# Kernel optimization log

Hardware: AMD Instinct MI355X
Metric: run time of the kernel (lower is better)

## Reference

```python
import jax, jax.numpy as jnp
import numpy as np

S, D, H, DK, DV = 4096, 1024, 16, 64, 64


def setup_inputs() -> dict:
    key = jax.random.key(0)
    ks = jax.random.split(key, 6)
    x = jax.random.normal(ks[0], (S, D), dtype=jnp.float32)
    # per-head projection weights, stacked over heads; scaled for numerical sanity
    Wq = jax.random.normal(ks[1], (H, D, DK), dtype=jnp.float32) / np.sqrt(D)
    Wk = jax.random.normal(ks[2], (H, D, DK), dtype=jnp.float32) / np.sqrt(D)
    Wv = jax.random.normal(ks[3], (H, D, DV), dtype=jnp.float32) / np.sqrt(D)
    Wc = jax.random.normal(ks[4], (H * DV, D), dtype=jnp.float32) / np.sqrt(H * DV)
    bc = jnp.zeros((D,), dtype=jnp.float32)
    return {"x": x, "Wq": Wq, "Wk": Wk, "Wv": Wv, "Wc": Wc, "bc": bc}


def reference(x, Wq, Wk, Wv, Wc, bc):
    # Per-head projections (original loops over heads with separate Linears;
    # stacking over h is the same math, vectorized).
    q = jnp.einsum("sd,hdk->hsk", x, Wq)   # [H,S,DK]
    k = jnp.einsum("sd,hdk->hsk", x, Wk)   # [H,S,DK]
    v = jnp.einsum("sd,hdv->hsv", x, Wv)   # [H,S,DV]
    scores = jnp.einsum("hsk,htk->hst", q, k) / jnp.sqrt(jnp.asarray(DK, x.dtype))
    probs = jax.nn.softmax(scores, axis=-1)  # softmax over last dim, per row
    o = jnp.einsum("hst,htv->hsv", probs, v)  # [H,S,DV]
    cat = jnp.transpose(o, (1, 0, 2)).reshape(S, H * DV)  # concat heads on last dim
    return cat @ Wc + bc  # output projection with bias
```

## Files before the change

kernel.cpp:

```cpp
#include <hip/hip_runtime.h>
#include <hip/hip_bf16.h>

#define S_ 4096
#define D_ 1024
#define H_ 16
#define DK_ 64
#define DV_ 64

typedef short bf16x8 __attribute__((ext_vector_type(8)));
typedef short bf16x4 __attribute__((ext_vector_type(4)));
typedef float floatx4 __attribute__((ext_vector_type(4)));
using bf16 = __hip_bfloat16;

#define MFMA16(a, b, c) __builtin_amdgcn_mfma_f32_16x16x32_bf16(a, b, c, 0, 0, 0)

#if __has_builtin(__builtin_amdgcn_exp2f)
#define EXP2(x) __builtin_amdgcn_exp2f(x)
#else
#define EXP2(x) exp2f(x)
#endif

__device__ __forceinline__ void stage16(const void* g, void* l) {
    __builtin_amdgcn_global_load_lds(
        (const __attribute__((address_space(1))) void*)g,
        (__attribute__((address_space(3))) void*)l, 16, 0, 0);
}

__device__ __forceinline__ bf16x8 ldsfrag(const bf16* base, int row, int chunk) {
    return *(const bf16x8*)(base + row * 64 + (((chunk ^ (row & 7))) << 3));
}
__device__ __forceinline__ bf16x8 ldsfrag32(const bf16* base, int row, int chunk) {
    return *(const bf16x8*)(base + row * 32 + (((chunk ^ (row & 3))) << 3));
}

__device__ __forceinline__ unsigned short bfbits(float f) {
    union { bf16 h; unsigned short u; } c; c.h = __float2bfloat16(f); return c.u;
}

__global__ __launch_bounds__(256)
void prep(const float* __restrict__ x, const float* __restrict__ Wq,
          const float* __restrict__ Wk, const float* __restrict__ Wv,
          const float* __restrict__ Wc,
          bf16* __restrict__ xb, bf16* __restrict__ Wt, bf16* __restrict__ Wct)
{
    __shared__ float ls[64][65];
    const int bx = blockIdx.x, t = threadIdx.x;

    if (bx < 2048) {
        int i = bx * 2048 + t * 8;
        float4 a = *(const float4*)(x + i);
        float4 b = *(const float4*)(x + i + 4);
        ushort4 lo, hi;
        lo.x = bfbits(a.x); lo.y = bfbits(a.y); lo.z = bfbits(a.z); lo.w = bfbits(a.w);
        hi.x = bfbits(b.x); hi.y = bfbits(b.y); hi.z = bfbits(b.z); hi.w = bfbits(b.w);
        *(ushort4*)(xb + i) = lo;
        *(ushort4*)(xb + i + 4) = hi;
        return;
    }
    if (bx < 2816) {
        const int idx = bx - 2048;
        const int z = idx >> 4, which = z >> 4, h = z & 15;
        const float* s = (which == 0 ? Wq : which == 1 ? Wk : Wv) + (size_t)h * D_ * 64;
        bf16* d = Wt + ((size_t)which * 1024 + h * 64) * D_;
        const float scale = (which == 0) ? 0.125f * 1.44269504088896340736f : 1.0f;
        const int r0 = (idx & 15) * 64;
        {
            int r = t >> 2, cseg = (t & 3) * 16;
            const float* sp = s + (size_t)(r0 + r) * 64 + cseg;
            #pragma unroll
            for (int i = 0; i < 16; i += 4) {
                float4 v = *(const float4*)(sp + i);
                ls[r][cseg + i + 0] = v.x; ls[r][cseg + i + 1] = v.y;
                ls[r][cseg + i + 2] = v.z; ls[r][cseg + i + 3] = v.w;
            }
        }
        __syncthreads();
        {
            int c = t >> 2, rseg = (t & 3) * 16;
            bf16* dp = d + (size_t)c * D_ + r0 + rseg;
            #pragma unroll
            for (int i = 0; i < 16; i++) dp[i] = __float2bfloat16(ls[rseg + i][c] * scale);
        }
        return;
    }
    {
        const int idx = bx - 2816;
        const int r0 = (idx & 15) * 64, c0 = (idx >> 4) * 64;
        {
            int r = t >> 2, cseg = (t & 3) * 16;
            const float* sp = Wc + (size_t)(r0 + r) * D_ + c0 + cseg;
            #pragma unroll
            for (int i = 0; i < 16; i += 4) {
                float4 v = *(const float4*)(sp + i);
                ls[r][cseg + i + 0] = v.x; ls[r][cseg + i + 1] = v.y;
                ls[r][cseg + i + 2] = v.z; ls[r][cseg + i + 3] = v.w;
            }
        }
        __syncthreads();
        {
            int c = t >> 2, rseg = (t & 3) * 16;
            bf16* dp = Wct + (size_t)(c0 + c) * D_ + r0 + rseg;
            #pragma unroll
            for (int i = 0; i < 16; i++) dp[i] = __float2bfloat16(ls[rseg + i][c]);
        }
    }
}

__global__ __launch_bounds__(256)
void qkv_gemm(const bf16* __restrict__ xb, const bf16* __restrict__ Wt,
              bf16* __restrict__ Qb, bf16* __restrict__ Kb, bf16* __restrict__ Vtb)
{
    const int m0 = blockIdx.x * 128;
    const int n0 = blockIdx.y * 128;
    __shared__ __align__(16) bf16 xa[2][128 * 32];
    __shared__ __align__(16) bf16 wb2[2][128 * 32];

    const int t = threadIdx.x, lane = t & 63, w = t >> 6;
    const int l15 = lane & 15, quad = lane >> 4;

    auto stage_a = [&](int buf, int kk) {
        #pragma unroll
        for (int j = 0; j < 2; j++) {
            int row = j * 64 + (t >> 2);
            int ch  = (t & 3) ^ (row & 3);
            stage16((const char*)xb + ((size_t)(m0 + row) * D_ + kk) * 2 + ch * 16,
                    (char*)&xa[buf][0] + (j * 4 + w) * 1024);
        }
    };
    auto stage_b = [&](int buf, int kk) {
        #pragma unroll
        for (int j = 0; j < 2; j++) {
            int row = j * 64 + (t >> 2);
            int ch  = (t & 3) ^ (row & 3);
            stage16((const char*)Wt + ((size_t)(n0 + row) * D_ + kk) * 2 + ch * 16,
                    (char*)&wb2[buf][0] + (j * 4 + w) * 1024);
        }
    };

    const floatx4 fz = {0.f, 0.f, 0.f, 0.f};
    floatx4 acc[2][8];
    #pragma unroll
    for (int mt = 0; mt < 2; mt++)
        #pragma unroll
        for (int nt = 0; nt < 8; nt++) acc[mt][nt] = fz;

    stage_a(0, 0); stage_b(0, 0);
    for (int kt = 0; kt < 32; kt++) {
        int cur = kt & 1;
        __syncthreads();
        if (kt < 31) { stage_a(cur ^ 1, (kt + 1) * 32); stage_b(cur ^ 1, (kt + 1) * 32); }
        bf16x8 a0 = ldsfrag32(&xa[cur][0], w * 32 + l15,      quad);
        bf16x8 a1 = ldsfrag32(&xa[cur][0], w * 32 + 16 + l15, quad);
        #pragma unroll
        for (int nt = 0; nt < 8; nt++) {
            bf16x8 b = ldsfrag32(&wb2[cur][0], nt * 16 + l15, quad);
            acc[0][nt] = MFMA16(a0, b, acc[0][nt]);
            acc[1][nt] = MFMA16(a1, b, acc[1][nt]);
        }
    }

    const int which = n0 >> 10;
    #pragma unroll
    for (int nt = 0; nt < 8; nt++) {
        int n = n0 + nt * 16 + l15;
        int hh = (n >> 6) & 15, col = n & 63;
        #pragma unroll
        for (int mt = 0; mt < 2; mt++)
            #pragma unroll
            for (int r = 0; r < 4; r++) {
                int s = m0 + w * 32 + mt * 16 + quad * 4 + r;
                bf16 val = __float2bfloat16(acc[mt][nt][r]);
                if (which == 0)      Qb[((size_t)hh * S_ + s) * 64 + col] = val;
                else if (which == 1) Kb[((size_t)hh * S_ + s) * 64 + col] = val;
                else                 Vtb[((size_t)hh * 64 + col) * S_ + s] = val;
            }
    }
}

template<int NKT, bool FULL>
__global__ __launch_bounds__(256, 4)
void attn(const bf16* __restrict__ Qb, const bf16* __restrict__ Kb,
          const bf16* __restrict__ Vtb, bf16* __restrict__ Cat,
          float* __restrict__ Opart, float* __restrict__ lpart)
{
    const int m0 = blockIdx.x * 128;
    const int h  = blockIdx.y;
    const int half = blockIdx.z;
    const int keybase = half * (NKT * 64);

    __shared__ __align__(16) bf16 ka[2][64 * 64];
    __shared__ __align__(16) bf16 vt[2][64 * 64];

    const int t = threadIdx.x, lane = t & 63, w = t >> 6;
    const int l15 = lane & 15, quad = lane >> 4;

    auto stage_kv = [&](int buf, int key0) {
        const char* kg = (const char*)(Kb + ((size_t)h * S_ + key0) * 64);
        #pragma unroll
        for (int j = 0; j < 2; j++) {
            int c = (j * 4 + w) * 64 + lane;
            int row = c >> 3, ch = (c & 7) ^ (row & 7);
            stage16(kg + row * 128 + ch * 16, (char*)&ka[buf][0] + (j * 4 + w) * 1024);
        }
        const char* vg = (const char*)(Vtb + (size_t)h * 64 * S_ + key0);
        #pragma unroll
        for (int j = 0; j < 2; j++) {
            int c = (j * 4 + w) * 64 + lane;
            int row = c >> 3, ch = (c & 7) ^ (row & 7);
            stage16(vg + (size_t)row * (S_ * 2) + ch * 16, (char*)&vt[buf][0] + (j * 4 + w) * 1024);
        }
    };

    bf16x8 qf[2][2];
    #pragma unroll
    for (int nq = 0; nq < 2; nq++)
        #pragma unroll
        for (int ks = 0; ks < 2; ks++)
            qf[nq][ks] = *(const bf16x8*)(Qb +
                ((size_t)h * S_ + m0 + w * 32 + nq * 16 + l15) * 64 + ks * 32 + quad * 8);

    const floatx4 fz = {0.f, 0.f, 0.f, 0.f};
    floatx4 acc[2][4];
    float rs[2] = {0.f, 0.f};
    #pragma unroll
    for (int nq = 0; nq < 2; nq++)
        #pragma unroll
        for (int nt = 0; nt < 4; nt++) acc[nq][nt] = fz;

    stage_kv(0, keybase);
    __syncthreads();

    for (int kt = 0; kt < NKT; kt++) {
        const int cur = kt & 1;
        if (kt + 1 < NKT) stage_kv(cur ^ 1, keybase + (kt + 1) * 64);

        floatx4 sc[4][2];
        #pragma unroll
        for (int mk = 0; mk < 4; mk++)
            #pragma unroll
            for (int nq = 0; nq < 2; nq++) sc[mk][nq] = fz;
        #pragma unroll
        for (int ks = 0; ks < 2; ks++) {
            bf16x8 af[4];
            #pragma unroll
            for (int mk = 0; mk < 4; mk++)
                af[mk] = ldsfrag(&ka[cur][0], mk * 16 + l15, ks * 4 + quad);
            #pragma unroll
            for (int mk = 0; mk < 4; mk++)
                #pragma unroll
                for (int nq = 0; nq < 2; nq++)
                    sc[mk][nq] = MFMA16(af[mk], qf[nq][ks], sc[mk][nq]);
        }

        bf16x4 pf[4][2];
        #pragma unroll
        for (int mk = 0; mk < 4; mk++)
            #pragma unroll
            for (int nq = 0; nq < 2; nq++) {
                float p0 = EXP2(sc[mk][nq][0]);
                float p1 = EXP2(sc[mk][nq][1]);
                float p2 = EXP2(sc[mk][nq][2]);
                float p3 = EXP2(sc[mk][nq][3]);
                rs[nq] += (p0 + p1) + (p2 + p3);
                union { bf16x4 v; unsigned short e[4]; } u;
                u.e[0] = bfbits(p0); u.e[1] = bfbits(p1);
                u.e[2] = bfbits(p2); u.e[3] = bfbits(p3);
                pf[mk][nq] = u.v;
            }

        #pragma unroll
        for (int p = 0; p < 2; p++) {
            union { bf16x8 v8; bf16x4 v4[2]; } b8[2];
            #pragma unroll
            for (int nq = 0; nq < 2; nq++) {
                b8[nq].v4[0] = pf[2 * p + 0][nq];
                b8[nq].v4[1] = pf[2 * p + 1][nq];
            }
            #pragma unroll
            for (int nt = 0; nt < 4; nt++) {
                const char* vb = (const char*)&vt[cur][0]
                               + (nt * 16 + l15) * 128 + (quad & 1) * 8;
                const int r7 = l15 & 7;
                union { bf16x8 v8; bf16x4 v4[2]; } a8;
                a8.v4[0] = *(const bf16x4*)(vb + (((4 * p +     (quad >> 1)) ^ r7) << 4));
                a8.v4[1] = *(const bf16x4*)(vb + (((4 * p + 2 + (quad >> 1)) ^ r7) << 4));
                #pragma unroll
                for (int nq = 0; nq < 2; nq++)
                    acc[nq][nt] = MFMA16(a8.v8, b8[nq].v8, acc[nq][nt]);
            }
        }
        __syncthreads();
    }

    #pragma unroll
    for (int nq = 0; nq < 2; nq++) {
        rs[nq] += __shfl_xor(rs[nq], 16);
        rs[nq] += __shfl_xor(rs[nq], 32);
    }

    if (FULL) {
        #pragma unroll
        for (int nq = 0; nq < 2; nq++) {
            float inv = 1.0f / rs[nq];
            int q = m0 + w * 32 + nq * 16 + l15;
            #pragma unroll
            for (int nt = 0; nt < 4; nt++) {
                ushort4 o;
                o.x = bfbits(acc[nq][nt][0] * inv);
                o.y = bfbits(acc[nq][nt][1] * inv);
                o.z = bfbits(acc[nq][nt][2] * inv);
                o.w = bfbits(acc[nq][nt][3] * inv);
                *(ushort4*)(Cat + (size_t)q * (H_ * DV_) + h * 64 + nt * 16 + quad * 4) = o;
            }
        }
    } else {
        const size_t plane = (size_t)(half * H_ + h) * S_;
        #pragma unroll
        for (int nq = 0; nq < 2; nq++) {
            int q = m0 + w * 32 + nq * 16 + l15;
            #pragma unroll
            for (int nt = 0; nt < 4; nt++) {
                float4 o = { acc[nq][nt][0], acc[nq][nt][1],
                             acc[nq][nt][2], acc[nq][nt][3] };
                *(float4*)(Opart + (plane + q) * 64 + nt * 16 + quad * 4) = o;
            }
            if (quad == 0) lpart[plane + q] = rs[nq];
        }
    }
}

__global__ __launch_bounds__(256)
void combine(const float* __restrict__ Opart, const float* __restrict__ lpart,
             bf16* __restrict__ Cat)
{
    const int h = blockIdx.y;
    const int off = blockIdx.x * 1024 + threadIdx.x * 4;
    const int s = off >> 6, dv = off & 63;
    float4 o0 = *(const float4*)(Opart + (size_t)h * S_ * 64 + off);
    float4 o1 = *(const float4*)(Opart + (size_t)(H_ + h) * S_ * 64 + off);
    float inv = 1.0f / (lpart[(size_t)h * S_ + s] + lpart[(size_t)(H_ + h) * S_ + s]);
    ushort4 o;
    o.x = bfbits((o0.x + o1.x) * inv);
    o.y = bfbits((o0.y + o1.y) * inv);
    o.z = bfbits((o0.z + o1.z) * inv);
    o.w = bfbits((o0.w + o1.w) * inv);
    *(ushort4*)(Cat + (size_t)s * (H_ * DV_) + h * 64 + dv) = o;
}

__global__ __launch_bounds__(256)
void out_proj(const bf16* __restrict__ Cat, const bf16* __restrict__ Wct,
              const float* __restrict__ bc, float* __restrict__ out)
{
    const int m0 = blockIdx.x * 128;
    const int n0 = blockIdx.y * 64;
    __shared__ __align__(16) bf16 ca[2][128 * 32];
    __shared__ __align__(16) bf16 wb2[2][64 * 32];

    const int t = threadIdx.x, lane = t & 63, w = t >> 6;
    const int l15 = lane & 15, quad = lane >> 4;

    auto stage_a = [&](int buf, int kk) {
        #pragma unroll
        for (int j = 0; j < 2; j++) {
            int row = j * 64 + (t >> 2);
            int ch  = (t & 3) ^ (row & 3);
            stage16((const char*)Cat + ((size_t)(m0 + row) * D_ + kk) * 2 + ch * 16,
                    (char*)&ca[buf][0] + (j * 4 + w) * 1024);
        }
    };
    auto stage_b = [&](int buf, int kk) {
        int row = t >> 2;
        int ch  = (t & 3) ^ (row & 3);
        stage16((const char*)Wct + ((size_t)(n0 + row) * D_ + kk) * 2 + ch * 16,
                (char*)&wb2[buf][0] + w * 1024);
    };

    const floatx4 fz = {0.f, 0.f, 0.f, 0.f};
    floatx4 acc[2][4];
    #pragma unroll
    for (int mt = 0; mt < 2; mt++)
        #pragma unroll
        for (int nt = 0; nt < 4; nt++) acc[mt][nt] = fz;

    stage_a(0, 0); stage_b(0, 0);
    for (int kt = 0; kt < 32; kt++) {
        int cur = kt & 1;
        __syncthreads();
        if (kt < 31) { stage_a(cur ^ 1, (kt + 1) * 32); stage_b(cur ^ 1, (kt + 1) * 32); }
        bf16x8 a0 = ldsfrag32(&ca[cur][0], w * 32 + l15,      quad);
        bf16x8 a1 = ldsfrag32(&ca[cur][0], w * 32 + 16 + l15, quad);
        #pragma unroll
        for (int nt = 0; nt < 4; nt++) {
            bf16x8 b = ldsfrag32(&wb2[cur][0], nt * 16 + l15, quad);
            acc[0][nt] = MFMA16(a0, b, acc[0][nt]);
            acc[1][nt] = MFMA16(a1, b, acc[1][nt]);
        }
    }

    #pragma unroll
    for (int nt = 0; nt < 4; nt++) {
        int col = n0 + nt * 16 + l15;
        float bias = bc[col];
        #pragma unroll
        for (int mt = 0; mt < 2; mt++)
            #pragma unroll
            for (int r = 0; r < 4; r++) {
                int row = m0 + w * 32 + mt * 16 + quad * 4 + r;
                out[(size_t)row * D_ + col] = acc[mt][nt][r] + bias;
            }
    }
}

extern "C" void kernel_launch(void* const* d_in, const int* in_sizes, int n_in,
                              void* d_out, int out_size, void* d_ws, size_t ws_size,
                              hipStream_t stream)
{
    const float* x  = (const float*)d_in[0];
    const float* Wq = (const float*)d_in[1];
    const float* Wk = (const float*)d_in[2];
    const float* Wv = (const float*)d_in[3];
    const float* Wc = (const float*)d_in[4];
    const float* bc = (const float*)d_in[5];
    float* out = (float*)d_out;

    bf16* xb  = (bf16*)d_ws;
    bf16* Cat = xb;
    bf16* Wt  = xb  + (size_t)S_ * D_;
    bf16* Wct = Wt  + (size_t)3 * H_ * 64 * D_;
    bf16* Qb  = Wct + (size_t)D_ * H_ * DV_;
    bf16* Kb  = Qb  + (size_t)H_ * S_ * 64;
    bf16* Vtb = Kb  + (size_t)H_ * S_ * 64;
    float* Opart = (float*)(Vtb + (size_t)H_ * 64 * S_);
    float* lpart = Opart + (size_t)2 * H_ * S_ * 64;

    const size_t need_split = (size_t)((char*)(lpart + (size_t)2 * H_ * S_) - (char*)d_ws);
    const bool split = ws_size >= need_split;

    prep<<<dim3(3072), 256, 0, stream>>>(x, Wq, Wk, Wv, Wc, xb, Wt, Wct);
    qkv_gemm<<<dim3(S_ / 128, 3072 / 128), 256, 0, stream>>>(xb, Wt, Qb, Kb, Vtb);

    if (split) {
        attn<32, false><<<dim3(S_ / 128, H_, 2), 256, 0, stream>>>(
            Qb, Kb, Vtb, Cat, Opart, lpart);
        combine<<<dim3(S_ * 64 / 1024, H_), 256, 0, stream>>>(Opart, lpart, Cat);
    } else {
        attn<64, true><<<dim3(S_ / 128, H_, 1), 256, 0, stream>>>(
            Qb, Kb, Vtb, Cat, Opart, lpart);
    }

    out_proj<<<dim3(S_ / 128, D_ / 64), 256, 0, stream>>>(Cat, Wct, bc, out);
}
```

Measured before the change: 241.3 us.

## Store split-attention partials in bf16, pack conversions, precompute LDS offsets

The split-key attention partial outputs are now written as bf16 instead of fp32, which halves the Opart traffic between attn and combine. The combine kernel is widened to 8 elements per thread to match. Scalar bf16 conversions are replaced with packed two-element conversions in prep, attn and combine. Per-iteration LDS swizzle offsets are precomputed once, and the zero-initialised score accumulators are folded into the first MFMA. Rounding the unnormalised partials to bf16 adds some error before the final sum.

```diff
diff --git a/kernel.cpp b/kernel.cpp
--- a/kernel.cpp
+++ b/kernel.cpp
@@ -36,6 +36,12 @@
 __device__ __forceinline__ unsigned short bfbits(float f) {
     union { bf16 h; unsigned short u; } c; c.h = __float2bfloat16(f); return c.u;
 }
+__device__ __forceinline__ float bf2f(bf16 h) { return __bfloat162float(h); }
+__device__ __forceinline__ unsigned int pkbf(float a, float b) {
+    union { __hip_bfloat162 h2; unsigned int u; } c;
+    c.h2 = __float22bfloat162_rn(float2{a, b});
+    return c.u;
+}
 
 __global__ __launch_bounds__(256)
 void prep(const float* __restrict__ x, const float* __restrict__ Wq,
@@ -50,11 +56,10 @@
         int i = bx * 2048 + t * 8;
         float4 a = *(const float4*)(x + i);
         float4 b = *(const float4*)(x + i + 4);
-        ushort4 lo, hi;
-        lo.x = bfbits(a.x); lo.y = bfbits(a.y); lo.z = bfbits(a.z); lo.w = bfbits(a.w);
-        hi.x = bfbits(b.x); hi.y = bfbits(b.y); hi.z = bfbits(b.z); hi.w = bfbits(b.w);
-        *(ushort4*)(xb + i) = lo;
-        *(ushort4*)(xb + i + 4) = hi;
+        uint4 o;
+        o.x = pkbf(a.x, a.y); o.y = pkbf(a.z, a.w);
+        o.z = pkbf(b.x, b.y); o.w = pkbf(b.z, b.w);
+        *(uint4*)(xb + i) = o;
         return;
     }
     if (bx < 2816) {
@@ -181,7 +186,7 @@
 __global__ __launch_bounds__(256, 4)
 void attn(const bf16* __restrict__ Qb, const bf16* __restrict__ Kb,
           const bf16* __restrict__ Vtb, bf16* __restrict__ Cat,
-          float* __restrict__ Opart, float* __restrict__ lpart)
+          bf16* __restrict__ Opart, float* __restrict__ lpart)
 {
     const int m0 = blockIdx.x * 128;
     const int h  = blockIdx.y;
@@ -219,6 +224,27 @@
             qf[nq][ks] = *(const bf16x8*)(Qb +
                 ((size_t)h * S_ + m0 + w * 32 + nq * 16 + l15) * 64 + ks * 32 + quad * 8);
 
+    int ka_off[8];
+    #pragma unroll
+    for (int ks = 0; ks < 2; ks++)
+        #pragma unroll
+        for (int mk = 0; mk < 4; mk++) {
+            int row = mk * 16 + l15, ch = ks * 4 + quad;
+            ka_off[ks * 4 + mk] = row * 128 + (((ch ^ (row & 7))) << 4);
+        }
+    int vt_off[2][4][2];
+    {
+        const int r7 = l15 & 7;
+        #pragma unroll
+        for (int p = 0; p < 2; p++)
+            #pragma unroll
+            for (int nt = 0; nt < 4; nt++) {
+                int base = (nt * 16 + l15) * 128 + (quad & 1) * 8;
+                vt_off[p][nt][0] = base + (((4 * p +     (quad >> 1)) ^ r7) << 4);
+                vt_off[p][nt][1] = base + (((4 * p + 2 + (quad >> 1)) ^ r7) << 4);
+            }
+    }
+
     const floatx4 fz = {0.f, 0.f, 0.f, 0.f};
     floatx4 acc[2][4];
     float rs[2] = {0.f, 0.f};
@@ -234,25 +260,26 @@
         const int cur = kt & 1;
         if (kt + 1 < NKT) stage_kv(cur ^ 1, keybase + (kt + 1) * 64);
 
+        const char* kab = (const char*)&ka[cur][0];
+        const char* vtb = (const char*)&vt[cur][0];
+
         floatx4 sc[4][2];
-        #pragma unroll
-        for (int mk = 0; mk < 4; mk++)
-            #pragma unroll
-            for (int nq = 0; nq < 2; nq++) sc[mk][nq] = fz;
         #pragma unroll
         for (int ks = 0; ks < 2; ks++) {
             bf16x8 af[4];
             #pragma unroll
             for (int mk = 0; mk < 4; mk++)
-                af[mk] = ldsfrag(&ka[cur][0], mk * 16 + l15, ks * 4 + quad);
+                af[mk] = *(const bf16x8*)(kab + ka_off[ks * 4 + mk]);
             #pragma unroll
             for (int mk = 0; mk < 4; mk++)
                 #pragma unroll
                 for (int nq = 0; nq < 2; nq++)
-                    sc[mk][nq] = MFMA16(af[mk], qf[nq][ks], sc[mk][nq]);
-        }
-
-        bf16x4 pf[4][2];
+                    sc[mk][nq] = MFMA16(af[mk], qf[nq][ks],
+                                        ks == 0 ? fz : sc[mk][nq]);
+        }
+
+        union bf4u { bf16x4 v; unsigned int u[2]; };
+        bf4u pf[4][2];
         #pragma unroll
         for (int mk = 0; mk < 4; mk++)
             #pragma unroll
@@ -262,10 +289,8 @@
                 float p2 = EXP2(sc[mk][nq][2]);
                 float p3 = EXP2(sc[mk][nq][3]);
                 rs[nq] += (p0 + p1) + (p2 + p3);
-                union { bf16x4 v; unsigned short e[4]; } u;
-                u.e[0] = bfbits(p0); u.e[1] = bfbits(p1);
-                u.e[2] = bfbits(p2); u.e[3] = bfbits(p3);
-                pf[mk][nq] = u.v;
+                pf[mk][nq].u[0] = pkbf(p0, p1);
+                pf[mk][nq].u[1] = pkbf(p2, p3);
             }
 
         #pragma unroll
@@ -273,17 +298,14 @@
             union { bf16x8 v8; bf16x4 v4[2]; } b8[2];
             #pragma unroll
             for (int nq = 0; nq < 2; nq++) {
-                b8[nq].v4[0] = pf[2 * p + 0][nq];
-                b8[nq].v4[1] = pf[2 * p + 1][nq];
+                b8[nq].v4[0] = pf[2 * p + 0][nq].v;
+                b8[nq].v4[1] = pf[2 * p + 1][nq].v;
             }
             #pragma unroll
             for (int nt = 0; nt < 4; nt++) {
-                const char* vb = (const char*)&vt[cur][0]
-                               + (nt * 16 + l15) * 128 + (quad & 1) * 8;
-                const int r7 = l15 & 7;
                 union { bf16x8 v8; bf16x4 v4[2]; } a8;
-                a8.v4[0] = *(const bf16x4*)(vb + (((4 * p +     (quad >> 1)) ^ r7) << 4));
-                a8.v4[1] = *(const bf16x4*)(vb + (((4 * p + 2 + (quad >> 1)) ^ r7) << 4));
+                a8.v4[0] = *(const bf16x4*)(vtb + vt_off[p][nt][0]);
+                a8.v4[1] = *(const bf16x4*)(vtb + vt_off[p][nt][1]);
                 #pragma unroll
                 for (int nq = 0; nq < 2; nq++)
                     acc[nq][nt] = MFMA16(a8.v8, b8[nq].v8, acc[nq][nt]);
@@ -305,12 +327,10 @@
             int q = m0 + w * 32 + nq * 16 + l15;
             #pragma unroll
             for (int nt = 0; nt < 4; nt++) {
-                ushort4 o;
-                o.x = bfbits(acc[nq][nt][0] * inv);
-                o.y = bfbits(acc[nq][nt][1] * inv);
-                o.z = bfbits(acc[nq][nt][2] * inv);
-                o.w = bfbits(acc[nq][nt][3] * inv);
-                *(ushort4*)(Cat + (size_t)q * (H_ * DV_) + h * 64 + nt * 16 + quad * 4) = o;
+                uint2 o;
+                o.x = pkbf(acc[nq][nt][0] * inv, acc[nq][nt][1] * inv);
+                o.y = pkbf(acc[nq][nt][2] * inv, acc[nq][nt][3] * inv);
+                *(uint2*)(Cat + (size_t)q * (H_ * DV_) + h * 64 + nt * 16 + quad * 4) = o;
             }
         }
     } else {
@@ -320,9 +340,10 @@
             int q = m0 + w * 32 + nq * 16 + l15;
             #pragma unroll
             for (int nt = 0; nt < 4; nt++) {
-                float4 o = { acc[nq][nt][0], acc[nq][nt][1],
-                             acc[nq][nt][2], acc[nq][nt][3] };
-                *(float4*)(Opart + (plane + q) * 64 + nt * 16 + quad * 4) = o;
+                uint2 o;
+                o.x = pkbf(acc[nq][nt][0], acc[nq][nt][1]);
+                o.y = pkbf(acc[nq][nt][2], acc[nq][nt][3]);
+                *(uint2*)(Opart + (plane + q) * 64 + nt * 16 + quad * 4) = o;
             }
             if (quad == 0) lpart[plane + q] = rs[nq];
         }
@@ -330,21 +351,22 @@
 }
 
 __global__ __launch_bounds__(256)
-void combine(const float* __restrict__ Opart, const float* __restrict__ lpart,
+void combine(const bf16* __restrict__ Opart, const float* __restrict__ lpart,
              bf16* __restrict__ Cat)
 {
     const int h = blockIdx.y;
-    const int off = blockIdx.x * 1024 + threadIdx.x * 4;
+    const int off = (blockIdx.x * 256 + threadIdx.x) * 8;
     const int s = off >> 6, dv = off & 63;
-    float4 o0 = *(const float4*)(Opart + (size_t)h * S_ * 64 + off);
-    float4 o1 = *(const float4*)(Opart + (size_t)(H_ + h) * S_ * 64 + off);
+    union { bf16x8 v; bf16 e[8]; } o0, o1;
+    o0.v = *(const bf16x8*)(Opart + (size_t)h * S_ * 64 + off);
+    o1.v = *(const bf16x8*)(Opart + (size_t)(H_ + h) * S_ * 64 + off);
     float inv = 1.0f / (lpart[(size_t)h * S_ + s] + lpart[(size_t)(H_ + h) * S_ + s]);
-    ushort4 o;
-    o.x = bfbits((o0.x + o1.x) * inv);
-    o.y = bfbits((o0.y + o1.y) * inv);
-    o.z = bfbits((o0.z + o1.z) * inv);
-    o.w = bfbits((o0.w + o1.w) * inv);
-    *(ushort4*)(Cat + (size_t)s * (H_ * DV_) + h * 64 + dv) = o;
+    uint4 o;
+    o.x = pkbf((bf2f(o0.e[0]) + bf2f(o1.e[0])) * inv, (bf2f(o0.e[1]) + bf2f(o1.e[1])) * inv);
+    o.y = pkbf((bf2f(o0.e[2]) + bf2f(o1.e[2])) * inv, (bf2f(o0.e[3]) + bf2f(o1.e[3])) * inv);
+    o.z = pkbf((bf2f(o0.e[4]) + bf2f(o1.e[4])) * inv, (bf2f(o0.e[5]) + bf2f(o1.e[5])) * inv);
+    o.w = pkbf((bf2f(o0.e[6]) + bf2f(o1.e[6])) * inv, (bf2f(o0.e[7]) + bf2f(o1.e[7])) * inv);
+    *(uint4*)(Cat + (size_t)s * (H_ * DV_) + h * 64 + dv) = o;
 }
 
 __global__ __launch_bounds__(256)
@@ -430,8 +452,8 @@
     bf16* Qb  = Wct + (size_t)D_ * H_ * DV_;
     bf16* Kb  = Qb  + (size_t)H_ * S_ * 64;
     bf16* Vtb = Kb  + (size_t)H_ * S_ * 64;
-    float* Opart = (float*)(Vtb + (size_t)H_ * 64 * S_);
-    float* lpart = Opart + (size_t)2 * H_ * S_ * 64;
+    bf16* Opart = Vtb + (size_t)H_ * 64 * S_;
+    float* lpart = (float*)(Opart + (size_t)2 * H_ * S_ * 64);
 
     const size_t need_split = (size_t)((char*)(lpart + (size_t)2 * H_ * S_) - (char*)d_ws);
     const bool split = ws_size >= need_split;
@@ -442,7 +464,7 @@
     if (split) {
         attn<32, false><<<dim3(S_ / 128, H_, 2), 256, 0, stream>>>(
             Qb, Kb, Vtb, Cat, Opart, lpart);
-        combine<<<dim3(S_ * 64 / 1024, H_), 256, 0, stream>>>(Opart, lpart, Cat);
+        combine<<<dim3(S_ * 64 / 2048, H_), 256, 0, stream>>>(Opart, lpart, Cat);
     } else {
         attn<64, true><<<dim3(S_ / 128, H_, 1), 256, 0, stream>>>(
             Qb, Kb, Vtb, Cat, Opart, lpart);
```

Result: slower. 248.0 us (+2.7%).
